# Performance work log

Measured on AMD Instinct MI355X. Metric: run time of the kernel, lower is better.

## Reference

```python
import jax, jax.numpy as jnp
import numpy as np

EPS = 1e-5  # torch LayerNorm default

def _layernorm(x, g, b):
    m = x.mean(-1, keepdims=True)
    v = ((x - m) ** 2).mean(-1, keepdims=True)
    return (x - m) * jax.lax.rsqrt(v + EPS) * g + b

def setup_inputs() -> dict:
    key = jax.random.key(0)
    ks = jax.random.split(key, 6)
    B, T, D, N, L = 16, 4096, 512, 77, 768
    s = 0.02
    return {
        "x": jax.random.normal(ks[0], (B, T, D), jnp.float32),
        "xf": jax.random.normal(ks[1], (B, N, L), jnp.float32),
        "q_w": jax.random.normal(ks[2], (D, D), jnp.float32) * s,
        "q_b": jnp.zeros((D,), jnp.float32),
        "k_w": jax.random.normal(ks[3], (D, L), jnp.float32) * s,
        "k_b": jnp.zeros((D,), jnp.float32),
        "v_w": jax.random.normal(ks[4], (D, L), jnp.float32) * s,
        "v_b": jnp.zeros((D,), jnp.float32),
        "norm_g": jnp.ones((D,), jnp.float32),
        "norm_b": jnp.zeros((D,), jnp.float32),
        "tnorm_g": jnp.ones((L,), jnp.float32),
        "tnorm_b": jnp.zeros((L,), jnp.float32),
        "num_heads": 8,
    }

def reference(x, xf, q_w, q_b, k_w, k_b, v_w, v_b, norm_g, norm_b, tnorm_g, tnorm_b, num_heads):
    B, T, D = x.shape
    N = xf.shape[1]
    H = num_heads
    xn = _layernorm(x, norm_g, norm_b)          # [B,T,D]
    xfn = _layernorm(xf, tnorm_g, tnorm_b)      # [B,N,L]
    # projections (torch Linear: y = x @ W^T + b)
    q = (xn @ q_w.T + q_b).reshape(B, T, H, -1)
    k = (xfn @ k_w.T + k_b).reshape(B, N, H, -1)
    v = (xfn @ v_w.T + v_b).reshape(B, N, H, -1)
    q = jax.nn.softmax(q, axis=-1)              # softmax over head feature dim
    k = jax.nn.softmax(k, axis=1)               # softmax over text token dim N
    # context: per-head [d,l] matrix, never materializes T x N scores
    att = jnp.einsum('bnhd,bnhl->bhdl', k, v)   # [B,H,d,l]
    y = jnp.einsum('bthd,bhdl->bthl', q, att).reshape(B, T, D)
    return x + y
```

## Files before the change

kernel.cpp:

```cpp
#include <hip/hip_runtime.h>

typedef __attribute__((ext_vector_type(8))) __bf16 bf16x8;
typedef __attribute__((ext_vector_type(4))) float f32x4;
typedef __attribute__((ext_vector_type(8))) unsigned short u16x8;
typedef __attribute__((ext_vector_type(4))) unsigned short u16x4;

#define MFMA16(a, b, c) __builtin_amdgcn_mfma_f32_16x16x32_bf16((a), (b), (c), 0, 0, 0)

static __device__ __forceinline__ unsigned short f2bf(float f) {
    union { float f; unsigned int u; } v;
    v.f = f;
    unsigned int r = v.u + 0x7FFFu + ((v.u >> 16) & 1u);
    return (unsigned short)(r >> 16);
}

__global__ __launch_bounds__(256) void prep_kernel(
    const float* __restrict__ qw, const float* __restrict__ kw,
    const float* __restrict__ vw,
    unsigned short* __restrict__ wfrag, unsigned short* __restrict__ kv_wf)
{
    const int idx = blockIdx.x * 256 + threadIdx.x;
    if (idx < 262144) {
        const int i = idx & 7, lane = (idx >> 3) & 63, kk = (idx >> 9) & 15, nb = idx >> 13;
        const int row = nb * 16 + (lane & 15);
        const int col = kk * 32 + ((lane >> 4) << 3) + i;
        wfrag[idx] = f2bf(qw[row * 512 + col]);
    } else {
        const int jdx = idx - 262144;
        const int i = jdx & 7, lane = (jdx >> 3) & 63;
        const int rest = jdx >> 9;
        const int kk = rest % 24, nb = rest / 24;
        const int j = nb * 16 + (lane & 15);
        const int k = kk * 32 + ((lane >> 4) << 3) + i;
        kv_wf[jdx] = f2bf(j < 512 ? kw[j * 768 + k] : vw[(j - 512) * 768 + k]);
    }
}

#define LDK 776
__global__ __launch_bounds__(256) void kv_kernel(
    const float* __restrict__ xf, const unsigned short* __restrict__ kv_wf,
    const float* __restrict__ kb, const float* __restrict__ vb,
    const float* __restrict__ tg, const float* __restrict__ tb,
    float* __restrict__ kv)
{
    __shared__ unsigned short xfn[80 * LDK];
    const int tid = threadIdx.x;
    const int lane = tid & 63;
    const int w = tid >> 6;
    const int l15 = lane & 15;
    const int lg = lane >> 4;
    const int b = blockIdx.y;
    const int jt = blockIdx.x;

    float g[12], be[12];
#pragma unroll
    for (int c = 0; c < 3; ++c) {
        const float4 gv = *(const float4*)(tg + c * 256 + lane * 4);
        const float4 bv = *(const float4*)(tb + c * 256 + lane * 4);
        g[c*4+0]=gv.x; g[c*4+1]=gv.y; g[c*4+2]=gv.z; g[c*4+3]=gv.w;
        be[c*4+0]=bv.x; be[c*4+1]=bv.y; be[c*4+2]=bv.z; be[c*4+3]=bv.w;
    }

    for (int n = w; n < 77; n += 4) {
        const float* xr = xf + (long)(b * 77 + n) * 768;
        float vals[12];
#pragma unroll
        for (int c = 0; c < 3; ++c) {
            const float4 v4 = *(const float4*)(xr + c * 256 + lane * 4);
            vals[c*4+0]=v4.x; vals[c*4+1]=v4.y; vals[c*4+2]=v4.z; vals[c*4+3]=v4.w;
        }
        float s = 0.f, ss = 0.f;
#pragma unroll
        for (int j = 0; j < 12; ++j) { s += vals[j]; ss += vals[j] * vals[j]; }
#pragma unroll
        for (int off = 32; off > 0; off >>= 1) {
            s += __shfl_xor(s, off);
            ss += __shfl_xor(ss, off);
        }
        const float mean = s * (1.f / 768.f);
        const float var = ss * (1.f / 768.f) - mean * mean;
        const float rstd = rsqrtf(var + 1e-5f);
#pragma unroll
        for (int c = 0; c < 3; ++c) {
            u16x4 o;
#pragma unroll
            for (int q = 0; q < 4; ++q)
                o[q] = f2bf((vals[c*4+q] - mean) * rstd * g[c*4+q] + be[c*4+q]);
            *(u16x4*)&xfn[n * LDK + c * 256 + lane * 4] = o;
        }
    }
    for (int idx = tid; idx < 3 * 768; idx += 256)
        xfn[(77 + idx / 768) * LDK + (idx % 768)] = 0;
    __syncthreads();

    const int nb = jt * 4 + w;
    f32x4 acc[5];
#pragma unroll
    for (int m = 0; m < 5; ++m) { acc[m][0]=0.f; acc[m][1]=0.f; acc[m][2]=0.f; acc[m][3]=0.f; }
    for (int kk = 0; kk < 24; ++kk) {
        const bf16x8 bw = *(const bf16x8*)&kv_wf[((nb * 24 + kk) * 64 + lane) * 8];
#pragma unroll
        for (int m = 0; m < 5; ++m) {
            const bf16x8 a = *(const bf16x8*)&xfn[(m * 16 + l15) * LDK + kk * 32 + lg * 8];
            acc[m] = MFMA16(a, bw, acc[m]);
        }
    }
    const int j = nb * 16 + l15;
    const float bias = (j < 512) ? kb[j] : vb[j - 512];
#pragma unroll
    for (int m = 0; m < 5; ++m) {
#pragma unroll
        for (int reg = 0; reg < 4; ++reg) {
            const int n = m * 16 + lg * 4 + reg;
            if (n < 77)
                kv[(long)(b * 77 + n) * 1024 + j] = acc[m][reg] + bias;
        }
    }
}

__global__ __launch_bounds__(256) void att_kernel(
    const float* __restrict__ kv, unsigned short* __restrict__ att_fr)
{
    const int b = blockIdx.x >> 3;
    const int h = blockIdx.x & 7;
    __shared__ float k_lds[77][65];
    __shared__ float v_lds[77][65];
    __shared__ float att_lds[64][65];
    const int tid = threadIdx.x;

    for (int idx = tid; idx < 77 * 64; idx += 256) {
        const int n = idx >> 6, d = idx & 63;
        const long base = (long)(b * 77 + n) * 1024 + h * 64 + d;
        k_lds[n][d] = kv[base];
        v_lds[n][d] = kv[base + 512];
    }
    __syncthreads();
    if (tid < 64) {
        float mx = -1e30f;
        for (int n = 0; n < 77; ++n) mx = fmaxf(mx, k_lds[n][tid]);
        float s = 0.f;
        for (int n = 0; n < 77; ++n) {
            const float e = __expf(k_lds[n][tid] - mx);
            k_lds[n][tid] = e;
            s += e;
        }
        const float inv = 1.f / s;
        for (int n = 0; n < 77; ++n) k_lds[n][tid] *= inv;
    }
    __syncthreads();
    {
        const int l = tid & 63, db = (tid >> 6) * 16;
        float a[16];
#pragma unroll
        for (int i = 0; i < 16; ++i) a[i] = 0.f;
        for (int n = 0; n < 77; ++n) {
            const float vv = v_lds[n][l];
#pragma unroll
            for (int i = 0; i < 16; ++i) a[i] += k_lds[n][db + i] * vv;
        }
#pragma unroll
        for (int i = 0; i < 16; ++i) att_lds[db + i][l] = a[i];
    }
    __syncthreads();
    const long hb8 = (long)(b * 8 + h) * 4096;
    for (int idx = tid; idx < 4096; idx += 256) {
        const int i = idx & 7, lane = (idx >> 3) & 63, kk = (idx >> 9) & 1, nf = (idx >> 10);
        const int d = kk * 32 + ((lane >> 4) << 3) + i;
        const int l = nf * 16 + (lane & 15);
        att_fr[hb8 + (long)(nf * 2 + kk) * 512 + lane * 8 + i] = f2bf(att_lds[d][l]);
    }
}

#define LDA 520
#define LDY 516

#define WLD(n, kk) (*(const bf16x8*)&wfrag[((((w * 4 + (n)) * 16 + (kk)) * 64) + lane) * 8])
#define ALD(m, kk) (*(const bf16x8*)&xn[((m) * 16 + l15) * LDA + (kk) * 32 + lg * 8])

__global__ __launch_bounds__(512, 4) void fused4(
    const float* __restrict__ x, const unsigned short* __restrict__ wfrag,
    const float* __restrict__ qb, const float* __restrict__ ng,
    const float* __restrict__ nbt, const unsigned short* __restrict__ att_fr,
    float* __restrict__ out)
{
    __shared__ char smem[64 * LDA * 2];
    unsigned short* const xn = (unsigned short*)smem;
    float* const ylds = (float*)smem;
    const int tid = threadIdx.x;
    const int lane = tid & 63;
    const int w = tid >> 6;
    const int l15 = lane & 15;
    const int lg = lane >> 4;
    const int b = blockIdx.y;
    const long rowbase = (long)b * 4096 + (long)blockIdx.x * 64;
    const float* xblk = x + rowbase * 512;

    float g[8], be[8];
    {
        const float4 g0 = *(const float4*)(ng + lane * 8);
        const float4 g1 = *(const float4*)(ng + lane * 8 + 4);
        const float4 b0 = *(const float4*)(nbt + lane * 8);
        const float4 b1 = *(const float4*)(nbt + lane * 8 + 4);
        g[0]=g0.x; g[1]=g0.y; g[2]=g0.z; g[3]=g0.w;
        g[4]=g1.x; g[5]=g1.y; g[6]=g1.z; g[7]=g1.w;
        be[0]=b0.x; be[1]=b0.y; be[2]=b0.z; be[3]=b0.w;
        be[4]=b1.x; be[5]=b1.y; be[6]=b1.z; be[7]=b1.w;
    }

    {
        float vals[8][8];
#pragma unroll
        for (int r = 0; r < 8; ++r) {
            const float* xr = xblk + (w * 8 + r) * 512 + lane * 8;
            const float4 v0 = *(const float4*)xr;
            const float4 v1 = *(const float4*)(xr + 4);
            vals[r][0]=v0.x; vals[r][1]=v0.y; vals[r][2]=v0.z; vals[r][3]=v0.w;
            vals[r][4]=v1.x; vals[r][5]=v1.y; vals[r][6]=v1.z; vals[r][7]=v1.w;
        }
#pragma unroll
        for (int r = 0; r < 8; ++r) {
            float s = 0.f, ss = 0.f;
#pragma unroll
            for (int j = 0; j < 8; ++j) { s += vals[r][j]; ss += vals[r][j] * vals[r][j]; }
#pragma unroll
            for (int off = 32; off > 0; off >>= 1) {
                s += __shfl_xor(s, off);
                ss += __shfl_xor(ss, off);
            }
            const float mean = s * (1.f / 512.f);
            const float var = ss * (1.f / 512.f) - mean * mean;
            const float rstd = rsqrtf(var + 1e-5f);
            u16x8 o;
#pragma unroll
            for (int j = 0; j < 8; ++j)
                o[j] = f2bf((vals[r][j] - mean) * rstd * g[j] + be[j]);
            *(u16x8*)&xn[(w * 8 + r) * LDA + lane * 8] = o;
        }
    }
    __syncthreads();

    const int wcol = w * 64;
    f32x4 acc[4][4];
#pragma unroll
    for (int n = 0; n < 4; ++n) {
        const float qbv = qb[wcol + n * 16 + l15];
#pragma unroll
        for (int m = 0; m < 4; ++m) {
            acc[m][n][0]=qbv; acc[m][n][1]=qbv; acc[m][n][2]=qbv; acc[m][n][3]=qbv;
        }
    }

    {
        bf16x8 aC[4], bC[4];
#pragma unroll
        for (int m = 0; m < 4; ++m) aC[m] = ALD(m, 0);
#pragma unroll
        for (int n = 0; n < 4; ++n) bC[n] = WLD(n, 0);
#pragma unroll
        for (int kk = 0; kk < 16; ++kk) {
            bf16x8 aN[4], bN[4];
            if (kk < 15) {
#pragma unroll
                for (int m = 0; m < 4; ++m) aN[m] = ALD(m, kk + 1);
#pragma unroll
                for (int n = 0; n < 4; ++n) bN[n] = WLD(n, kk + 1);
            }
#pragma unroll
            for (int n = 0; n < 4; ++n)
#pragma unroll
                for (int m = 0; m < 4; ++m)
                    acc[m][n] = MFMA16(aC[m], bC[n], acc[m][n]);
            if (kk < 15) {
#pragma unroll
                for (int m = 0; m < 4; ++m) aC[m] = aN[m];
#pragma unroll
                for (int n = 0; n < 4; ++n) bC[n] = bN[n];
            }
        }
    }

#pragma unroll
    for (int m = 0; m < 4; ++m) {
#pragma unroll
        for (int reg = 0; reg < 4; ++reg) {
            float mx = fmaxf(fmaxf(acc[m][0][reg], acc[m][1][reg]),
                             fmaxf(acc[m][2][reg], acc[m][3][reg]));
#pragma unroll
            for (int off = 1; off < 16; off <<= 1)
                mx = fmaxf(mx, __shfl_xor(mx, off));
            const float e0 = __expf(acc[m][0][reg] - mx);
            const float e1 = __expf(acc[m][1][reg] - mx);
            const float e2 = __expf(acc[m][2][reg] - mx);
            const float e3 = __expf(acc[m][3][reg] - mx);
            float sm = e0 + e1 + e2 + e3;
#pragma unroll
            for (int off = 1; off < 16; off <<= 1)
                sm += __shfl_xor(sm, off);
            const float inv = 1.f / sm;
            acc[m][0][reg] = e0 * inv;
            acc[m][1][reg] = e1 * inv;
            acc[m][2][reg] = e2 * inv;
            acc[m][3][reg] = e3 * inv;
        }
    }

    bf16x8 att_b[2][4];
#pragma unroll
    for (int kk = 0; kk < 2; ++kk)
#pragma unroll
        for (int nf = 0; nf < 4; ++nf)
            att_b[kk][nf] = *(const bf16x8*)&att_fr[
                (long)(b * 8 + w) * 4096 + (long)(nf * 2 + kk) * 512 + lane * 8];

    __syncthreads();

#pragma unroll
    for (int m = 0; m < 4; ++m)
#pragma unroll
        for (int n = 0; n < 4; ++n)
#pragma unroll
            for (int reg = 0; reg < 4; ++reg)
                xn[(m * 16 + lg * 4 + reg) * LDA + wcol + n * 16 + l15] =
                    f2bf(acc[m][n][reg]);

    f32x4 acc2[4][4];
#pragma unroll
    for (int m2 = 0; m2 < 4; ++m2)
#pragma unroll
        for (int nf = 0; nf < 4; ++nf) {
            acc2[m2][nf][0]=0.f; acc2[m2][nf][1]=0.f; acc2[m2][nf][2]=0.f; acc2[m2][nf][3]=0.f;
        }
#pragma unroll
    for (int kk = 0; kk < 2; ++kk) {
        bf16x8 a2[4];
#pragma unroll
        for (int m2 = 0; m2 < 4; ++m2)
            a2[m2] = *(const bf16x8*)&xn[(m2 * 16 + l15) * LDA + wcol + kk * 32 + lg * 8];
#pragma unroll
        for (int nf = 0; nf < 4; ++nf) {
#pragma unroll
            for (int m2 = 0; m2 < 4; ++m2)
                acc2[m2][nf] = MFMA16(a2[m2], att_b[kk][nf], acc2[m2][nf]);
        }
    }
    __syncthreads();

#pragma unroll
    for (int hh = 0; hh < 2; ++hh) {
#pragma unroll
        for (int m2h = 0; m2h < 2; ++m2h) {
            const int m2 = hh * 2 + m2h;
#pragma unroll
            for (int nf = 0; nf < 4; ++nf)
#pragma unroll
                for (int reg = 0; reg < 4; ++reg)
                    ylds[(m2h * 16 + lg * 4 + reg) * LDY + wcol + nf * 16 + l15] =
                        acc2[m2][nf][reg];
        }
        __syncthreads();
        const int row = tid >> 4;
        const long grow = rowbase + hh * 32 + row;
#pragma unroll
        for (int j = 0; j < 8; ++j) {
            const int col = j * 64 + (tid & 15) * 4;
            const float4 yv = *(const float4*)&ylds[row * LDY + col];
            const long gi = grow * 512 + col;
            const float4 xv = *(const float4*)&x[gi];
            float4 ov;
            ov.x = xv.x + yv.x; ov.y = xv.y + yv.y;
            ov.z = xv.z + yv.z; ov.w = xv.w + yv.w;
            *(float4*)&out[gi] = ov;
        }
        __syncthreads();
    }
}

extern "C" void kernel_launch(void* const* d_in, const int* in_sizes, int n_in,
                              void* d_out, int out_size, void* d_ws, size_t ws_size,
                              hipStream_t stream) {
    const float* x  = (const float*)d_in[0];
    const float* xf = (const float*)d_in[1];
    const float* qw = (const float*)d_in[2];
    const float* qb = (const float*)d_in[3];
    const float* kw = (const float*)d_in[4];
    const float* kb = (const float*)d_in[5];
    const float* vw = (const float*)d_in[6];
    const float* vb = (const float*)d_in[7];
    const float* ng = (const float*)d_in[8];
    const float* nb = (const float*)d_in[9];
    const float* tg = (const float*)d_in[10];
    const float* tb = (const float*)d_in[11];
    float* out = (float*)d_out;

    char* ws = (char*)d_ws;
    unsigned short* wfrag  = (unsigned short*)(ws);
    unsigned short* kv_wf  = (unsigned short*)(ws + 524288);
    float*          kv     = (float*)(ws + 2097152);
    unsigned short* att_fr = (unsigned short*)(ws + 7143424);

    prep_kernel<<<dim3(4096), dim3(256), 0, stream>>>(qw, kw, vw, wfrag, kv_wf);
    kv_kernel<<<dim3(16, 16), dim3(256), 0, stream>>>(xf, kv_wf, kb, vb, tg, tb, kv);
    att_kernel<<<dim3(128), dim3(256), 0, stream>>>(kv, att_fr);
    fused4<<<dim3(64, 16), dim3(512), 0, stream>>>(x, wfrag, qb, ng, nb, att_fr, out);
}
```

Before: 144.9 us.

## Halve fused tile to 32 rows and stage output through bf16 LDS

```diff
diff --git a/kernel.cpp b/kernel.cpp
--- a/kernel.cpp
+++ b/kernel.cpp
@@ -12,6 +12,11 @@
     v.f = f;
     unsigned int r = v.u + 0x7FFFu + ((v.u >> 16) & 1u);
     return (unsigned short)(r >> 16);
+}
+static __device__ __forceinline__ float bf2f(unsigned short u) {
+    union { unsigned int u; float f; } v;
+    v.u = ((unsigned int)u) << 16;
+    return v.f;
 }
 
 __global__ __launch_bounds__(256) void prep_kernel(
@@ -172,27 +177,24 @@
 }
 
 #define LDA 520
-#define LDY 516
 
 #define WLD(n, kk) (*(const bf16x8*)&wfrag[((((w * 4 + (n)) * 16 + (kk)) * 64) + lane) * 8])
 #define ALD(m, kk) (*(const bf16x8*)&xn[((m) * 16 + l15) * LDA + (kk) * 32 + lg * 8])
 
-__global__ __launch_bounds__(512, 4) void fused4(
+__global__ __launch_bounds__(512, 8) void fused5(
     const float* __restrict__ x, const unsigned short* __restrict__ wfrag,
     const float* __restrict__ qb, const float* __restrict__ ng,
     const float* __restrict__ nbt, const unsigned short* __restrict__ att_fr,
     float* __restrict__ out)
 {
-    __shared__ char smem[64 * LDA * 2];
-    unsigned short* const xn = (unsigned short*)smem;
-    float* const ylds = (float*)smem;
+    __shared__ unsigned short xn[32 * LDA];
     const int tid = threadIdx.x;
     const int lane = tid & 63;
     const int w = tid >> 6;
     const int l15 = lane & 15;
     const int lg = lane >> 4;
     const int b = blockIdx.y;
-    const long rowbase = (long)b * 4096 + (long)blockIdx.x * 64;
+    const long rowbase = (long)b * 4096 + (long)blockIdx.x * 32;
     const float* xblk = x + rowbase * 512;
 
     float g[8], be[8];
@@ -208,17 +210,17 @@
     }
 
     {
-        float vals[8][8];
-#pragma unroll
-        for (int r = 0; r < 8; ++r) {
-            const float* xr = xblk + (w * 8 + r) * 512 + lane * 8;
+        float vals[4][8];
+#pragma unroll
+        for (int r = 0; r < 4; ++r) {
+            const float* xr = xblk + (w * 4 + r) * 512 + lane * 8;
             const float4 v0 = *(const float4*)xr;
             const float4 v1 = *(const float4*)(xr + 4);
             vals[r][0]=v0.x; vals[r][1]=v0.y; vals[r][2]=v0.z; vals[r][3]=v0.w;
             vals[r][4]=v1.x; vals[r][5]=v1.y; vals[r][6]=v1.z; vals[r][7]=v1.w;
         }
 #pragma unroll
-        for (int r = 0; r < 8; ++r) {
+        for (int r = 0; r < 4; ++r) {
             float s = 0.f, ss = 0.f;
 #pragma unroll
             for (int j = 0; j < 8; ++j) { s += vals[r][j]; ss += vals[r][j] * vals[r][j]; }
@@ -234,45 +236,44 @@
 #pragma unroll
             for (int j = 0; j < 8; ++j)
                 o[j] = f2bf((vals[r][j] - mean) * rstd * g[j] + be[j]);
-            *(u16x8*)&xn[(w * 8 + r) * LDA + lane * 8] = o;
+            *(u16x8*)&xn[(w * 4 + r) * LDA + lane * 8] = o;
         }
     }
     __syncthreads();
 
     const int wcol = w * 64;
-    f32x4 acc[4][4];
+    f32x4 acc[2][4];
 #pragma unroll
     for (int n = 0; n < 4; ++n) {
         const float qbv = qb[wcol + n * 16 + l15];
 #pragma unroll
-        for (int m = 0; m < 4; ++m) {
+        for (int m = 0; m < 2; ++m) {
             acc[m][n][0]=qbv; acc[m][n][1]=qbv; acc[m][n][2]=qbv; acc[m][n][3]=qbv;
         }
     }
-
     {
-        bf16x8 aC[4], bC[4];
-#pragma unroll
-        for (int m = 0; m < 4; ++m) aC[m] = ALD(m, 0);
+        bf16x8 aC[2], bC[4];
+#pragma unroll
+        for (int m = 0; m < 2; ++m) aC[m] = ALD(m, 0);
 #pragma unroll
         for (int n = 0; n < 4; ++n) bC[n] = WLD(n, 0);
 #pragma unroll
         for (int kk = 0; kk < 16; ++kk) {
-            bf16x8 aN[4], bN[4];
+            bf16x8 aN[2], bN[4];
             if (kk < 15) {
 #pragma unroll
-                for (int m = 0; m < 4; ++m) aN[m] = ALD(m, kk + 1);
+                for (int m = 0; m < 2; ++m) aN[m] = ALD(m, kk + 1);
 #pragma unroll
                 for (int n = 0; n < 4; ++n) bN[n] = WLD(n, kk + 1);
             }
 #pragma unroll
             for (int n = 0; n < 4; ++n)
 #pragma unroll
-                for (int m = 0; m < 4; ++m)
+                for (int m = 0; m < 2; ++m)
                     acc[m][n] = MFMA16(aC[m], bC[n], acc[m][n]);
             if (kk < 15) {
 #pragma unroll
-                for (int m = 0; m < 4; ++m) aC[m] = aN[m];
+                for (int m = 0; m < 2; ++m) aC[m] = aN[m];
 #pragma unroll
                 for (int n = 0; n < 4; ++n) bC[n] = bN[n];
             }
@@ -280,7 +281,7 @@
     }
 
 #pragma unroll
-    for (int m = 0; m < 4; ++m) {
+    for (int m = 0; m < 2; ++m) {
 #pragma unroll
         for (int reg = 0; reg < 4; ++reg) {
             float mx = fmaxf(fmaxf(acc[m][0][reg], acc[m][1][reg]),
@@ -315,7 +316,7 @@
     __syncthreads();
 
 #pragma unroll
-    for (int m = 0; m < 4; ++m)
+    for (int m = 0; m < 2; ++m)
 #pragma unroll
         for (int n = 0; n < 4; ++n)
 #pragma unroll
@@ -323,55 +324,55 @@
                 xn[(m * 16 + lg * 4 + reg) * LDA + wcol + n * 16 + l15] =
                     f2bf(acc[m][n][reg]);
 
-    f32x4 acc2[4][4];
-#pragma unroll
-    for (int m2 = 0; m2 < 4; ++m2)
+    f32x4 acc2[2][4];
+#pragma unroll
+    for (int m2 = 0; m2 < 2; ++m2)
 #pragma unroll
         for (int nf = 0; nf < 4; ++nf) {
             acc2[m2][nf][0]=0.f; acc2[m2][nf][1]=0.f; acc2[m2][nf][2]=0.f; acc2[m2][nf][3]=0.f;
         }
 #pragma unroll
     for (int kk = 0; kk < 2; ++kk) {
-        bf16x8 a2[4];
-#pragma unroll
-        for (int m2 = 0; m2 < 4; ++m2)
+        bf16x8 a2[2];
+#pragma unroll
+        for (int m2 = 0; m2 < 2; ++m2)
             a2[m2] = *(const bf16x8*)&xn[(m2 * 16 + l15) * LDA + wcol + kk * 32 + lg * 8];
 #pragma unroll
         for (int nf = 0; nf < 4; ++nf) {
 #pragma unroll
-            for (int m2 = 0; m2 < 4; ++m2)
+            for (int m2 = 0; m2 < 2; ++m2)
                 acc2[m2][nf] = MFMA16(a2[m2], att_b[kk][nf], acc2[m2][nf]);
         }
     }
-    __syncthreads();
-
-#pragma unroll
-    for (int hh = 0; hh < 2; ++hh) {
-#pragma unroll
-        for (int m2h = 0; m2h < 2; ++m2h) {
-            const int m2 = hh * 2 + m2h;
-#pragma unroll
-            for (int nf = 0; nf < 4; ++nf)
-#pragma unroll
-                for (int reg = 0; reg < 4; ++reg)
-                    ylds[(m2h * 16 + lg * 4 + reg) * LDY + wcol + nf * 16 + l15] =
-                        acc2[m2][nf][reg];
-        }
-        __syncthreads();
+
+#pragma unroll
+    for (int m2 = 0; m2 < 2; ++m2)
+#pragma unroll
+        for (int nf = 0; nf < 4; ++nf)
+#pragma unroll
+            for (int reg = 0; reg < 4; ++reg)
+                xn[(m2 * 16 + lg * 4 + reg) * LDA + wcol + nf * 16 + l15] =
+                    f2bf(acc2[m2][nf][reg]);
+    __syncthreads();
+
+    {
         const int row = tid >> 4;
-        const long grow = rowbase + hh * 32 + row;
-#pragma unroll
-        for (int j = 0; j < 8; ++j) {
-            const int col = j * 64 + (tid & 15) * 4;
-            const float4 yv = *(const float4*)&ylds[row * LDY + col];
+        const long grow = rowbase + row;
+#pragma unroll
+        for (int j = 0; j < 4; ++j) {
+            const int col = j * 128 + (tid & 15) * 8;
+            const u16x8 yv = *(const u16x8*)&xn[row * LDA + col];
             const long gi = grow * 512 + col;
-            const float4 xv = *(const float4*)&x[gi];
-            float4 ov;
-            ov.x = xv.x + yv.x; ov.y = xv.y + yv.y;
-            ov.z = xv.z + yv.z; ov.w = xv.w + yv.w;
-            *(float4*)&out[gi] = ov;
-        }
-        __syncthreads();
+            const float4 x0 = *(const float4*)&x[gi];
+            const float4 x1 = *(const float4*)&x[gi + 4];
+            float4 o0, o1;
+            o0.x = x0.x + bf2f(yv[0]); o0.y = x0.y + bf2f(yv[1]);
+            o0.z = x0.z + bf2f(yv[2]); o0.w = x0.w + bf2f(yv[3]);
+            o1.x = x1.x + bf2f(yv[4]); o1.y = x1.y + bf2f(yv[5]);
+            o1.z = x1.z + bf2f(yv[6]); o1.w = x1.w + bf2f(yv[7]);
+            *(float4*)&out[gi] = o0;
+            *(float4*)&out[gi + 4] = o1;
+        }
     }
 }
 
@@ -401,5 +402,5 @@
     prep_kernel<<<dim3(4096), dim3(256), 0, stream>>>(qw, kw, vw, wfrag, kv_wf);
     kv_kernel<<<dim3(16, 16), dim3(256), 0, stream>>>(xf, kv_wf, kb, vb, tg, tb, kv);
     att_kernel<<<dim3(128), dim3(256), 0, stream>>>(kv, att_fr);
-    fused4<<<dim3(64, 16), dim3(512), 0, stream>>>(x, wfrag, qb, ng, nb, att_fr, out);
-}
+    fused5<<<dim3(128, 16), dim3(512), 0, stream>>>(x, wfrag, qb, ng, nb, att_fr, out);
+}
```

Result: slower. 172.7 us (+19.2%).

## Fold LayerNorm affine into Q weights and reuse x registers for residual

Applied to the files above, without the earlier changes.

```diff
diff --git a/kernel.cpp b/kernel.cpp
--- a/kernel.cpp
+++ b/kernel.cpp
@@ -16,7 +16,7 @@
 
 __global__ __launch_bounds__(256) void prep_kernel(
     const float* __restrict__ qw, const float* __restrict__ kw,
-    const float* __restrict__ vw,
+    const float* __restrict__ vw, const float* __restrict__ ng,
     unsigned short* __restrict__ wfrag, unsigned short* __restrict__ kv_wf)
 {
     const int idx = blockIdx.x * 256 + threadIdx.x;
@@ -24,7 +24,7 @@
         const int i = idx & 7, lane = (idx >> 3) & 63, kk = (idx >> 9) & 15, nb = idx >> 13;
         const int row = nb * 16 + (lane & 15);
         const int col = kk * 32 + ((lane >> 4) << 3) + i;
-        wfrag[idx] = f2bf(qw[row * 512 + col]);
+        wfrag[idx] = f2bf(qw[row * 512 + col] * ng[col]);
     } else {
         const int jdx = idx - 262144;
         const int i = jdx & 7, lane = (jdx >> 3) & 63;
@@ -34,6 +34,16 @@
         const int k = kk * 32 + ((lane >> 4) << 3) + i;
         kv_wf[jdx] = f2bf(j < 512 ? kw[j * 768 + k] : vw[(j - 512) * 768 + k]);
     }
+}
+
+__global__ __launch_bounds__(512) void qbias_kernel(
+    const float* __restrict__ qw, const float* __restrict__ qb,
+    const float* __restrict__ nbt, float* __restrict__ qb2)
+{
+    const int j = threadIdx.x;
+    float s = qb[j];
+    for (int k = 0; k < 512; ++k) s += nbt[k] * qw[j * 512 + k];
+    qb2[j] = s;
 }
 
 #define LDK 776
@@ -177,10 +187,9 @@
 #define WLD(n, kk) (*(const bf16x8*)&wfrag[((((w * 4 + (n)) * 16 + (kk)) * 64) + lane) * 8])
 #define ALD(m, kk) (*(const bf16x8*)&xn[((m) * 16 + l15) * LDA + (kk) * 32 + lg * 8])
 
-__global__ __launch_bounds__(512, 4) void fused4(
+__global__ __launch_bounds__(512, 4) void fused6(
     const float* __restrict__ x, const unsigned short* __restrict__ wfrag,
-    const float* __restrict__ qb, const float* __restrict__ ng,
-    const float* __restrict__ nbt, const unsigned short* __restrict__ att_fr,
+    const float* __restrict__ qb2, const unsigned short* __restrict__ att_fr,
     float* __restrict__ out)
 {
     __shared__ char smem[64 * LDA * 2];
@@ -191,50 +200,46 @@
     const int w = tid >> 6;
     const int l15 = lane & 15;
     const int lg = lane >> 4;
+    const int c16 = lane & 15;
+    const int rsub = lane >> 4;
+    const int row_local = w * 4 + rsub;
     const int b = blockIdx.y;
     const long rowbase = (long)b * 4096 + (long)blockIdx.x * 64;
-    const float* xblk = x + rowbase * 512;
-
-    float g[8], be[8];
-    {
-        const float4 g0 = *(const float4*)(ng + lane * 8);
-        const float4 g1 = *(const float4*)(ng + lane * 8 + 4);
-        const float4 b0 = *(const float4*)(nbt + lane * 8);
-        const float4 b1 = *(const float4*)(nbt + lane * 8 + 4);
-        g[0]=g0.x; g[1]=g0.y; g[2]=g0.z; g[3]=g0.w;
-        g[4]=g1.x; g[5]=g1.y; g[6]=g1.z; g[7]=g1.w;
-        be[0]=b0.x; be[1]=b0.y; be[2]=b0.z; be[3]=b0.w;
-        be[4]=b1.x; be[5]=b1.y; be[6]=b1.z; be[7]=b1.w;
-    }
-
-    {
-        float vals[8][8];
-#pragma unroll
-        for (int r = 0; r < 8; ++r) {
-            const float* xr = xblk + (w * 8 + r) * 512 + lane * 8;
-            const float4 v0 = *(const float4*)xr;
-            const float4 v1 = *(const float4*)(xr + 4);
-            vals[r][0]=v0.x; vals[r][1]=v0.y; vals[r][2]=v0.z; vals[r][3]=v0.w;
-            vals[r][4]=v1.x; vals[r][5]=v1.y; vals[r][6]=v1.z; vals[r][7]=v1.w;
-        }
-#pragma unroll
-        for (int r = 0; r < 8; ++r) {
-            float s = 0.f, ss = 0.f;
-#pragma unroll
-            for (int j = 0; j < 8; ++j) { s += vals[r][j]; ss += vals[r][j] * vals[r][j]; }
-#pragma unroll
-            for (int off = 32; off > 0; off >>= 1) {
-                s += __shfl_xor(s, off);
-                ss += __shfl_xor(ss, off);
-            }
-            const float mean = s * (1.f / 512.f);
-            const float var = ss * (1.f / 512.f) - mean * mean;
-            const float rstd = rsqrtf(var + 1e-5f);
-            u16x8 o;
-#pragma unroll
-            for (int j = 0; j < 8; ++j)
-                o[j] = f2bf((vals[r][j] - mean) * rstd * g[j] + be[j]);
-            *(u16x8*)&xn[(w * 8 + r) * LDA + lane * 8] = o;
+
+    float4 xr[2][8];
+#pragma unroll
+    for (int hh = 0; hh < 2; ++hh)
+#pragma unroll
+        for (int j = 0; j < 8; ++j)
+            xr[hh][j] = *(const float4*)&x[
+                (rowbase + hh * 32 + row_local) * 512 + c16 * 4 + j * 64];
+
+#pragma unroll
+    for (int hh = 0; hh < 2; ++hh) {
+        float s = 0.f, ss = 0.f;
+#pragma unroll
+        for (int j = 0; j < 8; ++j) {
+            const float4 v = xr[hh][j];
+            s += v.x + v.y + v.z + v.w;
+            ss += v.x * v.x + v.y * v.y + v.z * v.z + v.w * v.w;
+        }
+#pragma unroll
+        for (int off = 1; off < 16; off <<= 1) {
+            s += __shfl_xor(s, off);
+            ss += __shfl_xor(ss, off);
+        }
+        const float mean = s * (1.f / 512.f);
+        const float var = ss * (1.f / 512.f) - mean * mean;
+        const float rstd = rsqrtf(var + 1e-5f);
+#pragma unroll
+        for (int j = 0; j < 8; ++j) {
+            const float4 v = xr[hh][j];
+            u16x4 o;
+            o[0] = f2bf((v.x - mean) * rstd);
+            o[1] = f2bf((v.y - mean) * rstd);
+            o[2] = f2bf((v.z - mean) * rstd);
+            o[3] = f2bf((v.w - mean) * rstd);
+            *(u16x4*)&xn[(hh * 32 + row_local) * LDA + c16 * 4 + j * 64] = o;
         }
     }
     __syncthreads();
@@ -243,13 +248,12 @@
     f32x4 acc[4][4];
 #pragma unroll
     for (int n = 0; n < 4; ++n) {
-        const float qbv = qb[wcol + n * 16 + l15];
+        const float qbv = qb2[wcol + n * 16 + l15];
 #pragma unroll
         for (int m = 0; m < 4; ++m) {
             acc[m][n][0]=qbv; acc[m][n][1]=qbv; acc[m][n][2]=qbv; acc[m][n][3]=qbv;
         }
     }
-
     {
         bf16x8 aC[4], bC[4];
 #pragma unroll
@@ -358,18 +362,15 @@
                         acc2[m2][nf][reg];
         }
         __syncthreads();
-        const int row = tid >> 4;
-        const long grow = rowbase + hh * 32 + row;
+        const long grow = rowbase + hh * 32 + row_local;
 #pragma unroll
         for (int j = 0; j < 8; ++j) {
-            const int col = j * 64 + (tid & 15) * 4;
-            const float4 yv = *(const float4*)&ylds[row * LDY + col];
-            const long gi = grow * 512 + col;
-            const float4 xv = *(const float4*)&x[gi];
+            const float4 yv = *(const float4*)&ylds[row_local * LDY + c16 * 4 + j * 64];
+            const float4 xv = xr[hh][j];
             float4 ov;
             ov.x = xv.x + yv.x; ov.y = xv.y + yv.y;
             ov.z = xv.z + yv.z; ov.w = xv.w + yv.w;
-            *(float4*)&out[gi] = ov;
+            *(float4*)&out[grow * 512 + c16 * 4 + j * 64] = ov;
         }
         __syncthreads();
     }
@@ -397,9 +398,11 @@
     unsigned short* kv_wf  = (unsigned short*)(ws + 524288);
     float*          kv     = (float*)(ws + 2097152);
     unsigned short* att_fr = (unsigned short*)(ws + 7143424);
-
-    prep_kernel<<<dim3(4096), dim3(256), 0, stream>>>(qw, kw, vw, wfrag, kv_wf);
+    float*          qb2    = (float*)(ws + 8388608);
+
+    prep_kernel<<<dim3(4096), dim3(256), 0, stream>>>(qw, kw, vw, ng, wfrag, kv_wf);
+    qbias_kernel<<<dim3(1), dim3(512), 0, stream>>>(qw, qb, nb, qb2);
     kv_kernel<<<dim3(16, 16), dim3(256), 0, stream>>>(xf, kv_wf, kb, vb, tg, tb, kv);
     att_kernel<<<dim3(128), dim3(256), 0, stream>>>(kv, att_fr);
-    fused4<<<dim3(64, 16), dim3(512), 0, stream>>>(x, wfrag, qb, ng, nb, att_fr, out);
-}
+    fused6<<<dim3(64, 16), dim3(512), 0, stream>>>(x, wfrag, qb2, att_fr, out);
+}
```

Result: slower. 201.3 us (+38.9%).
